# Performance work log

Hardware: AMD Instinct MI355X
Metric: run time of the kernel (lower is better)

## Reference

```python
import jax, jax.numpy as jnp
import numpy as np

EPS = 1e-9
TOP_K = 2


def setup_inputs() -> dict:
    key = jax.random.key(0)
    k = jax.random.split(key, 6)
    B, E, D_IN, D_MODEL, D_SEL = 16384, 8, 900, 512, 128
    return {
        "cycle_curve_data": jax.random.normal(k[0], (B, D_IN), jnp.float32),
        "logits": jax.random.normal(k[1], (B, E), jnp.float32),
        "moe_masks": jax.random.randint(k[2], (B, E), 0, 2, jnp.int32),
        "selection_embeddings": jax.random.normal(k[3], (B, E, D_SEL), jnp.float32),
        "W": jax.random.normal(k[4], (E, D_IN, D_MODEL), jnp.float32) / np.sqrt(D_IN).astype(np.float32),
        "b": jnp.zeros((E, D_MODEL), jnp.float32),
    }


def reference(cycle_curve_data, logits, moe_masks, selection_embeddings, W, b):
    B, E = logits.shape
    mask = (moe_masks == 1).astype(logits.dtype)  # [B, E]
    raw = jax.nn.softmax(logits, axis=1)          # [B, E]

    # inactive-expert mixture for selection embedding
    inactive = raw * (1.0 - mask)
    inactive = inactive / (jnp.sum(inactive, axis=1, keepdims=True) + EPS)
    selection_embedding = jnp.einsum("bes,be->bs", selection_embeddings, inactive)

    # active gates + top-k selection + renormalization
    active = raw * mask
    _, idx = jax.lax.top_k(active, TOP_K)                                  # [B, K]
    top_mask = jnp.sum(jax.nn.one_hot(idx, E, dtype=active.dtype), axis=1)  # [B, E]
    gates = active * top_mask
    gates = gates / (jnp.sum(gates, axis=1, keepdims=True) + EPS)

    # dense formulation of dispatch -> per-expert Linear -> weighted combine:
    # out[b] = sum_e gates[b,e] * (x[b] @ W[e] + b[e])
    expert_out = jnp.einsum("bd,edm->bem", cycle_curve_data, W) + b  # [B, E, D_model]
    final_out = jnp.einsum("bem,be->bm", expert_out, gates).astype(jnp.bfloat16)

    # guide loss (training-mode auxiliary loss)
    s = jnp.sum(raw * mask) / B
    guide_loss = (1.0 - s) * (1.0 - s)
    return final_out, guide_loss, selection_embedding
```

## Files before the change

### kernel.cpp

```cpp
#include <hip/hip_runtime.h>
#include <hip/hip_bf16.h>


#define B_ROWS 16384
#define DIN 900
#define DM 512
#define DSEL 128
#define KP 928
#define NKS 29
#define MAXT 192
#define EPSF 1e-9f

#define OUT_GUIDE (B_ROWS*DM)
#define OUT_SEL   (B_ROWS*DM + 1)

#define WS_COUNTS 0
#define WS_PART   512
#define WS_NT     768
#define WS_OFF    1024
#define WS_ENT    2048
#define WS_BB     9216
#define WS_PIDLR  25600
#define WS_GATEB  91136
#define WS_W8     222208
#define WS_ROWSS  746496
#define WS_WT     812032

#define FRSTRIDE 14848

typedef __attribute__((ext_vector_type(8))) short short8;
typedef __attribute__((ext_vector_type(8))) unsigned short ushort8;
typedef __attribute__((ext_vector_type(4))) float floatx4;

__device__ inline unsigned short f2bf(float v){
  union { __hip_bfloat16 h; unsigned short u; } c;
  c.h = __float2bfloat16(v);
  return c.u;
}
__device__ inline float bf2f(unsigned short u){
  union { unsigned int i; float f; } c;
  c.i = ((unsigned int)u) << 16;
  return c.f;
}
__device__ inline short8 pack8(float4 a, float4 b){
  union { ushort8 u; short8 s; } c;
  c.u[0]=f2bf(a.x); c.u[1]=f2bf(a.y); c.u[2]=f2bf(a.z); c.u[3]=f2bf(a.w);
  c.u[4]=f2bf(b.x); c.u[5]=f2bf(b.y); c.u[6]=f2bf(b.z); c.u[7]=f2bf(b.w);
  return c.s;
}

__global__ __launch_bounds__(256) void cvtw2_k(const float* __restrict__ W,
                                               unsigned short* __restrict__ wt2){
  __shared__ unsigned short lds[32][512];
  int t = threadIdx.x;
  int kc = blockIdx.x, e = blockIdx.y;
  for (int kk = 0; kk < 32; ++kk){
    int k = kc*32 + kk;
    if (k < DIN){
      const float* wr = W + ((size_t)e*DIN + k)*DM;
      lds[kk][t]       = f2bf(wr[t]);
      lds[kk][t + 256] = f2bf(wr[t + 256]);
    } else {
      lds[kk][t] = 0; lds[kk][t + 256] = 0;
    }
  }
  __syncthreads();
  int ncg = t >> 3, q = t & 7;
  unsigned short* ob = wt2 + (((size_t)e*32 + ncg)*29 + kc)*512;
  for (int i = 0; i < 8; ++i){
    int fb = i*64 + q*8;
    int col = fb >> 5, kk0 = fb & 31;
    ushort8 y;
    #pragma unroll
    for (int j = 0; j < 8; ++j) y[j] = lds[kk0 + j][ncg*16 + col];
    *((ushort8*)(ob + fb)) = y;
  }
}

__global__ __launch_bounds__(256) void gating_k(const float* __restrict__ logits,
                                                const int* __restrict__ masks,
                                                int* __restrict__ counts,
                                                float* __restrict__ partials,
                                                int* __restrict__ pidlr,
                                                float2* __restrict__ gatesb,
                                                float* __restrict__ w8,
                                                int* __restrict__ blockbase){
  __shared__ int hist[64];
  __shared__ float wsum[4];
  int t = threadIdx.x;
  if (t < 64) hist[t] = 0;
  __syncthreads();
  int b = blockIdx.x*256 + t;
  float4 l0 = *(const float4*)&logits[(size_t)b*8];
  float4 l1 = *(const float4*)&logits[(size_t)b*8 + 4];
  int4  m0 = *(const int4*)&masks[(size_t)b*8];
  int4  m1 = *(const int4*)&masks[(size_t)b*8 + 4];
  float raw[8] = {l0.x,l0.y,l0.z,l0.w,l1.x,l1.y,l1.z,l1.w};
  int   mk[8]  = {m0.x,m0.y,m0.z,m0.w,m1.x,m1.y,m1.z,m1.w};
  float mx = raw[0];
  for (int e = 1; e < 8; e++) mx = fmaxf(mx, raw[e]);
  float Z = 0.f;
  for (int e = 0; e < 8; e++){ raw[e] = expf(raw[e]-mx); Z += raw[e]; }
  float invZ = 1.f/Z;
  float act[8], ina[8]; float srm = 0.f, isum = 0.f;
  for (int e = 0; e < 8; e++){
    raw[e] *= invZ;
    if (mk[e] == 1){ act[e] = raw[e]; ina[e] = 0.f; srm += raw[e]; }
    else           { act[e] = 0.f;    ina[e] = raw[e]; isum += raw[e]; }
  }
  float v1 = -1.f, v2 = -1.f; int e1 = 0, e2 = 0;
  for (int e = 0; e < 8; e++){
    float a = act[e];
    if (a > v1){ v2 = v1; e2 = e1; v1 = a; e1 = e; }
    else if (a > v2){ v2 = a; e2 = e; }
  }
  float den = v1 + v2 + EPSF;
  float g1 = v1/den, g2 = v2/den;
  int lo, hi; float gl, gh;
  if (e1 < e2){ lo = e1; hi = e2; gl = g1; gh = g2; }
  else        { lo = e2; hi = e1; gl = g2; gh = g1; }
  int pid = lo*8 + hi;
  float invI = 1.f/(isum + EPSF);
  for (int e = 0; e < 8; e++) w8[(size_t)b*8 + e] = ina[e]*invI;
  gatesb[b] = make_float2(gl, gh);
  int lr = atomicAdd(&hist[pid], 1);
  pidlr[b] = pid | (lr << 8);
  float s = srm;
  for (int sft = 32; sft > 0; sft >>= 1) s += __shfl_down(s, sft, 64);
  if ((t & 63) == 0) wsum[t >> 6] = s;
  __syncthreads();
  if (t < 64){
    int c = hist[t];
    int base = 0;
    if (c > 0) base = atomicAdd(&counts[t], c);
    blockbase[blockIdx.x*64 + t] = base;
  }
  if (t == 0) partials[blockIdx.x] = wsum[0] + wsum[1] + wsum[2] + wsum[3];
}

__global__ __launch_bounds__(256) void selemb_k(const float* __restrict__ sel,
                                                const float* __restrict__ w8,
                                                const int* __restrict__ pidlr,
                                                const int* __restrict__ off,
                                                const int* __restrict__ blockbase,
                                                int* __restrict__ rows_s,
                                                float* __restrict__ out){
  int t = threadIdx.x;
  int b = blockIdx.x*2 + (t >> 7);
  int d = t & 127;
  if (d == 0){
    int pl = pidlr[b];
    int p = pl & 63;
    int lr = pl >> 8;
    rows_s[off[p] + blockbase[(b >> 8)*64 + p] + lr] = b;
  }
  const float* wr = w8 + (size_t)b*8;
  const float* sb = sel + (size_t)b*(8*DSEL);
  float a = 0.f;
  for (int e = 0; e < 8; e++) a += wr[e] * sb[e*DSEL + d];
  out[OUT_SEL + (size_t)b*DSEL + d] = a;
}

__global__ void worklist_k(const int* __restrict__ counts,
                           const float* __restrict__ partials,
                           int* __restrict__ off, int* __restrict__ ntp,
                           int4* __restrict__ entries,
                           float* __restrict__ out){
  int lane = threadIdx.x;
  int c = counts[lane];
  int sc = c;
  for (int s = 1; s < 64; s <<= 1){ int v = __shfl_up(sc, s, 64); if (lane >= s) sc += v; }
  int offp = sc - c;
  off[lane] = offp;
  int nt = (c + 127) >> 7;
  int snt = nt;
  for (int s = 1; s < 64; s <<= 1){ int v = __shfl_up(snt, s, 64); if (lane >= s) snt += v; }
  int tbase = snt - nt;
  int elo = lane >> 3, ehi = lane & 7;
  for (int j = 0; j < nt; ++j){
    int nr = c - j*128; if (nr > 128) nr = 128;
    entries[tbase + j] = make_int4(elo, ehi, offp + j*128, nr);
  }
  int tot = __shfl(snt, 63, 64);
  if (lane == 0) *ntp = tot;
  float p = partials[lane];
  for (int s = 32; s > 0; s >>= 1) p += __shfl_down(p, s, 64);
  if (lane == 0){
    float sv = p * (1.f/B_ROWS);
    float d = 1.f - sv;
    out[OUT_GUIDE] = d*d;
  }
}


#define LDRAW(kks) { \
  r0 = *(const float4*)(ap0 + (kks)*32); r1 = *(const float4*)(ap0 + (kks)*32 + 4); \
  r2 = *(const float4*)(ap1 + (kks)*32); r3 = *(const float4*)(ap1 + (kks)*32 + 4); \
  r4 = *(const float4*)(ap2 + (kks)*32); r5 = *(const float4*)(ap2 + (kks)*32 + 4); \
  r6 = *(const float4*)(ap3 + (kks)*32); r7 = *(const float4*)(ap3 + (kks)*32 + 4); }

#define LDRAW_TAIL() { \
  float4 z = make_float4(0.f,0.f,0.f,0.f); \
  float4 t0 = *(const float4*)(ap0 - quad*8 + 896); \
  float4 t1 = *(const float4*)(ap1 - quad*8 + 896); \
  float4 t2 = *(const float4*)(ap2 - quad*8 + 896); \
  float4 t3 = *(const float4*)(ap3 - quad*8 + 896); \
  r0 = (quad==0)? t0 : z; r1 = z; \
  r2 = (quad==0)? t1 : z; r3 = z; \
  r4 = (quad==0)? t2 : z; r5 = z; \
  r6 = (quad==0)? t3 : z; r7 = z; }

#define CVT(dst) { \
  dst##0 = pack8(r0, r1); dst##1 = pack8(r2, r3); \
  dst##2 = pack8(r4, r5); dst##3 = pack8(r6, r7); }

#define MF(afX, b, ei, nt) { \
  acc[ei][0][nt] = __builtin_amdgcn_mfma_f32_16x16x32_bf16(afX##0, b, acc[ei][0][nt], 0, 0, 0); \
  acc[ei][1][nt] = __builtin_amdgcn_mfma_f32_16x16x32_bf16(afX##1, b, acc[ei][1][nt], 0, 0, 0); \
  acc[ei][2][nt] = __builtin_amdgcn_mfma_f32_16x16x32_bf16(afX##2, b, acc[ei][2][nt], 0, 0, 0); \
  acc[ei][3][nt] = __builtin_amdgcn_mfma_f32_16x16x32_bf16(afX##3, b, acc[ei][3][nt], 0, 0, 0); }

#define STEP(afX, kks, LASTF) { \
  short8 b0n, b1n; \
   \
  b0n = *((const short8*)(bp0 + 1*FRSTRIDE + (kks)*512)); \
  b1n = *((const short8*)(bp1 + 1*FRSTRIDE + (kks)*512)); \
  MF(afX, b0c, 0, 0); MF(afX, b1c, 1, 0); b0c = b0n; b1c = b1n; \
   \
  b0n = *((const short8*)(bp0 + 2*FRSTRIDE + (kks)*512)); \
  b1n = *((const short8*)(bp1 + 2*FRSTRIDE + (kks)*512)); \
  MF(afX, b0c, 0, 1); MF(afX, b1c, 1, 1); b0c = b0n; b1c = b1n; \
   \
  b0n = *((const short8*)(bp0 + 3*FRSTRIDE + (kks)*512)); \
  b1n = *((const short8*)(bp1 + 3*FRSTRIDE + (kks)*512)); \
  MF(afX, b0c, 0, 2); MF(afX, b1c, 1, 2); b0c = b0n; b1c = b1n; \
   \
  if (!(LASTF)){ \
    b0n = *((const short8*)(bp0 + ((kks)+1)*512)); \
    b1n = *((const short8*)(bp1 + ((kks)+1)*512)); \
  } \
  MF(afX, b0c, 0, 3); MF(afX, b1c, 1, 3); b0c = b0n; b1c = b1n; }

__global__ __launch_bounds__(256, 2) void gemm_k(const float* __restrict__ xf,
                                                 const unsigned short* __restrict__ wt2,
                                                 const float* __restrict__ bias,
                                                 const int* __restrict__ ntp,
                                                 const int4* __restrict__ entries,
                                                 const int* __restrict__ rows_s,
                                                 const float2* __restrict__ gatesb,
                                                 float* __restrict__ out){
  int tile = blockIdx.x;
  if (tile >= *ntp) return;
  int4 ent = entries[tile];
  int elo = ent.x, ehi = ent.y, start = ent.z, nrows = ent.w;

  int t = threadIdx.x, lane = t & 63, wid = t >> 6;
  int wrow = wid >> 1, wcol = wid & 1;
  int quad = lane >> 4, l16 = lane & 15;
  int ncg0 = blockIdx.y*8 + wcol*4;

  const float* ap0; const float* ap1; const float* ap2; const float* ap3;
  {
    int rr, g;
    rr = wrow*64 + 0*16 + l16; g = (rr < nrows) ? rows_s[start + rr] : 0;
    ap0 = xf + (size_t)g*DIN + quad*8;
    rr = wrow*64 + 1*16 + l16; g = (rr < nrows) ? rows_s[start + rr] : 0;
    ap1 = xf + (size_t)g*DIN + quad*8;
    rr = wrow*64 + 2*16 + l16; g = (rr < nrows) ? rows_s[start + rr] : 0;
    ap2 = xf + (size_t)g*DIN + quad*8;
    rr = wrow*64 + 3*16 + l16; g = (rr < nrows) ? rows_s[start + rr] : 0;
    ap3 = xf + (size_t)g*DIN + quad*8;
  }
  const unsigned short* bp0 = wt2 + ((size_t)(elo*32 + ncg0)*29)*512 + l16*32 + quad*8;
  const unsigned short* bp1 = wt2 + ((size_t)(ehi*32 + ncg0)*29)*512 + l16*32 + quad*8;

  floatx4 acc[2][4][4];
  #pragma unroll
  for (int i = 0; i < 2; i++)
    #pragma unroll
    for (int j = 0; j < 4; j++)
      #pragma unroll
      for (int k = 0; k < 4; k++)
        #pragma unroll
        for (int r = 0; r < 4; r++) acc[i][j][k][r] = 0.f;

  float4 r0,r1,r2,r3,r4,r5,r6,r7;
  short8 afA0, afA1, afA2, afA3;
  short8 afB0, afB1, afB2, afB3;

  LDRAW(0);
  CVT(afA);
  short8 b0c = *((const short8*)(bp0));
  short8 b1c = *((const short8*)(bp1));

  for (int ks = 0; ks < 28; ks += 2){
    LDRAW(ks+1);
    STEP(afA, ks, false);
    CVT(afB);
    if (ks + 2 < 28){ LDRAW(ks+2); } else { LDRAW_TAIL(); }
    STEP(afB, ks+1, false);
    CVT(afA);
  }
  STEP(afA, 28, true);

  float blo[4], bhi[4];
  #pragma unroll
  for (int nt = 0; nt < 4; ++nt){
    int n = (ncg0 + nt)*16 + l16;
    blo[nt] = bias[elo*DM + n];
    bhi[nt] = bias[ehi*DM + n];
  }
  #pragma unroll
  for (int mt = 0; mt < 4; ++mt){
    #pragma unroll
    for (int r = 0; r < 4; ++r){
      int rr = wrow*64 + mt*16 + quad*4 + r;
      if (rr < nrows){
        int grow = rows_s[start + rr];
        float2 gg = gatesb[grow];
        float* orow = out + (size_t)grow*DM;
        #pragma unroll
        for (int nt = 0; nt < 4; ++nt){
          int n = (ncg0 + nt)*16 + l16;
          float v = gg.x*(acc[0][mt][nt][r] + blo[nt]) + gg.y*(acc[1][mt][nt][r] + bhi[nt]);
          orow[n] = bf2f(f2bf(v));
        }
      }
    }
  }
}

extern "C" void kernel_launch(void* const* d_in, const int* in_sizes, int n_in,
                              void* d_out, int out_size, void* d_ws, size_t ws_size,
                              hipStream_t stream){
  const float* x      = (const float*)d_in[0];
  const float* logits = (const float*)d_in[1];
  const int*   masks  = (const int*)d_in[2];
  const float* sel    = (const float*)d_in[3];
  const float* W      = (const float*)d_in[4];
  const float* bias   = (const float*)d_in[5];
  float* out = (float*)d_out;
  char* ws = (char*)d_ws;
  int*    counts   = (int*)(ws + WS_COUNTS);
  float*  partials = (float*)(ws + WS_PART);
  int*    ntp      = (int*)(ws + WS_NT);
  int*    off      = (int*)(ws + WS_OFF);
  int4*   entries  = (int4*)(ws + WS_ENT);
  int*    blockbase= (int*)(ws + WS_BB);
  int*    pidlr    = (int*)(ws + WS_PIDLR);
  float2* gatesb   = (float2*)(ws + WS_GATEB);
  float*  w8       = (float*)(ws + WS_W8);
  int*    rows_s   = (int*)(ws + WS_ROWSS);
  unsigned short* wt2 = (unsigned short*)(ws + WS_WT);

  hipMemsetAsync(ws, 0, 256, stream);
  cvtw2_k<<<dim3(29, 8), 256, 0, stream>>>(W, wt2);
  gating_k<<<B_ROWS/256, 256, 0, stream>>>(logits, masks, counts, partials, pidlr, gatesb, w8, blockbase);
  worklist_k<<<1, 64, 0, stream>>>(counts, partials, off, ntp, entries, out);
  selemb_k<<<B_ROWS/2, 256, 0, stream>>>(sel, w8, pidlr, off, blockbase, rows_s, out);
  gemm_k<<<dim3(MAXT, 4), 256, 0, stream>>>(x, wt2, bias, ntp, entries, rows_s, gatesb, out);
}
```

Baseline: 332.6 us.

## Stage A and B tiles through double-buffered LDS in expert GEMM

Rewrites the grouped-expert GEMM main loop. Each thread used to load its own A rows and B fragments straight from global memory, so waves sharing a tile fetched the same data separately. Now the block loads x rows (converted to bf16) and weight fragments cooperatively into padded, double-buffered shared memory, with one barrier per k-step, and each wave reads its MFMA operands from LDS. Gather indices and gates are cached in shared memory. This removes redundant global traffic, at the cost of LDS footprint, barrier stalls and possibly lower occupancy.

```diff
diff --git a/kernel.cpp b/kernel.cpp
--- a/kernel.cpp
+++ b/kernel.cpp
@@ -26,8 +26,6 @@
 #define WS_ROWSS  746496
 #define WS_WT     812032
 
-#define FRSTRIDE 14848
-
 typedef __attribute__((ext_vector_type(8))) short short8;
 typedef __attribute__((ext_vector_type(8))) unsigned short ushort8;
 typedef __attribute__((ext_vector_type(4))) float floatx4;
@@ -42,11 +40,11 @@
   c.i = ((unsigned int)u) << 16;
   return c.f;
 }
-__device__ inline short8 pack8(float4 a, float4 b){
-  union { ushort8 u; short8 s; } c;
-  c.u[0]=f2bf(a.x); c.u[1]=f2bf(a.y); c.u[2]=f2bf(a.z); c.u[3]=f2bf(a.w);
-  c.u[4]=f2bf(b.x); c.u[5]=f2bf(b.y); c.u[6]=f2bf(b.z); c.u[7]=f2bf(b.w);
-  return c.s;
+__device__ inline ushort8 pack8u(float4 a, float4 b){
+  ushort8 c;
+  c[0]=f2bf(a.x); c[1]=f2bf(a.y); c[2]=f2bf(a.z); c[3]=f2bf(a.w);
+  c[4]=f2bf(b.x); c[5]=f2bf(b.y); c[6]=f2bf(b.z); c[7]=f2bf(b.w);
+  return c;
 }
 
 __global__ __launch_bounds__(256) void cvtw2_k(const float* __restrict__ W,
@@ -193,53 +191,38 @@
 }
 
 
-#define LDRAW(kks) { \
-  r0 = *(const float4*)(ap0 + (kks)*32); r1 = *(const float4*)(ap0 + (kks)*32 + 4); \
-  r2 = *(const float4*)(ap1 + (kks)*32); r3 = *(const float4*)(ap1 + (kks)*32 + 4); \
-  r4 = *(const float4*)(ap2 + (kks)*32); r5 = *(const float4*)(ap2 + (kks)*32 + 4); \
-  r6 = *(const float4*)(ap3 + (kks)*32); r7 = *(const float4*)(ap3 + (kks)*32 + 4); }
-
-#define LDRAW_TAIL() { \
-  float4 z = make_float4(0.f,0.f,0.f,0.f); \
-  float4 t0 = *(const float4*)(ap0 - quad*8 + 896); \
-  float4 t1 = *(const float4*)(ap1 - quad*8 + 896); \
-  float4 t2 = *(const float4*)(ap2 - quad*8 + 896); \
-  float4 t3 = *(const float4*)(ap3 - quad*8 + 896); \
-  r0 = (quad==0)? t0 : z; r1 = z; \
-  r2 = (quad==0)? t1 : z; r3 = z; \
-  r4 = (quad==0)? t2 : z; r5 = z; \
-  r6 = (quad==0)? t3 : z; r7 = z; }
-
-#define CVT(dst) { \
-  dst##0 = pack8(r0, r1); dst##1 = pack8(r2, r3); \
-  dst##2 = pack8(r4, r5); dst##3 = pack8(r6, r7); }
-
-#define MF(afX, b, ei, nt) { \
-  acc[ei][0][nt] = __builtin_amdgcn_mfma_f32_16x16x32_bf16(afX##0, b, acc[ei][0][nt], 0, 0, 0); \
-  acc[ei][1][nt] = __builtin_amdgcn_mfma_f32_16x16x32_bf16(afX##1, b, acc[ei][1][nt], 0, 0, 0); \
-  acc[ei][2][nt] = __builtin_amdgcn_mfma_f32_16x16x32_bf16(afX##2, b, acc[ei][2][nt], 0, 0, 0); \
-  acc[ei][3][nt] = __builtin_amdgcn_mfma_f32_16x16x32_bf16(afX##3, b, acc[ei][3][nt], 0, 0, 0); }
-
-#define STEP(afX, kks, LASTF) { \
-  short8 b0n, b1n; \
-   \
-  b0n = *((const short8*)(bp0 + 1*FRSTRIDE + (kks)*512)); \
-  b1n = *((const short8*)(bp1 + 1*FRSTRIDE + (kks)*512)); \
-  MF(afX, b0c, 0, 0); MF(afX, b1c, 1, 0); b0c = b0n; b1c = b1n; \
-   \
-  b0n = *((const short8*)(bp0 + 2*FRSTRIDE + (kks)*512)); \
-  b1n = *((const short8*)(bp1 + 2*FRSTRIDE + (kks)*512)); \
-  MF(afX, b0c, 0, 1); MF(afX, b1c, 1, 1); b0c = b0n; b1c = b1n; \
-   \
-  b0n = *((const short8*)(bp0 + 3*FRSTRIDE + (kks)*512)); \
-  b1n = *((const short8*)(bp1 + 3*FRSTRIDE + (kks)*512)); \
-  MF(afX, b0c, 0, 2); MF(afX, b1c, 1, 2); b0c = b0n; b1c = b1n; \
-   \
-  if (!(LASTF)){ \
-    b0n = *((const short8*)(bp0 + ((kks)+1)*512)); \
-    b1n = *((const short8*)(bp1 + ((kks)+1)*512)); \
-  } \
-  MF(afX, b0c, 0, 3); MF(afX, b1c, 1, 3); b0c = b0n; b1c = b1n; }
+#define ALOAD(kk) { \
+  if ((kk) < 28){ \
+    const float4* p = (const float4*)(xrow + (kk)*32); \
+    a0 = p[0]; a1 = p[1]; a2 = p[2]; a3 = p[3]; \
+  } else { \
+    float tmp[16]; \
+    _Pragma("unroll") \
+    for (int j = 0; j < 16; ++j){ \
+      int k = (kk)*32 + skc*16 + j; \
+      tmp[j] = (k < DIN) ? xrow[(kk)*32 + j] : 0.f; \
+    } \
+    a0 = make_float4(tmp[0],tmp[1],tmp[2],tmp[3]); \
+    a1 = make_float4(tmp[4],tmp[5],tmp[6],tmp[7]); \
+    a2 = make_float4(tmp[8],tmp[9],tmp[10],tmp[11]); \
+    a3 = make_float4(tmp[12],tmp[13],tmp[14],tmp[15]); \
+  } }
+
+#define BLOAD(kk) { \
+  bw0 = *((const ushort8*)(bg0 + (size_t)(kk)*512)); \
+  bw1 = *((const ushort8*)(bg1 + (size_t)(kk)*512)); \
+  bw2 = *((const ushort8*)(bg2 + (size_t)(kk)*512)); \
+  bw3 = *((const ushort8*)(bg3 + (size_t)(kk)*512)); }
+
+#define AWRITE(buf) { \
+  *((ushort8*)&as_[buf][srow*40 + skc*16])     = pack8u(a0, a1); \
+  *((ushort8*)&as_[buf][srow*40 + skc*16 + 8]) = pack8u(a2, a3); }
+
+#define BWRITE(buf) { \
+  *((ushort8*)&bs_[buf][bl0]) = bw0; \
+  *((ushort8*)&bs_[buf][bl1]) = bw1; \
+  *((ushort8*)&bs_[buf][bl2]) = bw2; \
+  *((ushort8*)&bs_[buf][bl3]) = bw3; }
 
 __global__ __launch_bounds__(256, 2) void gemm_k(const float* __restrict__ xf,
                                                  const unsigned short* __restrict__ wt2,
@@ -254,25 +237,48 @@
   int4 ent = entries[tile];
   int elo = ent.x, ehi = ent.y, start = ent.z, nrows = ent.w;
 
-  int t = threadIdx.x, lane = t & 63, wid = t >> 6;
+  __shared__ __align__(16) unsigned short as_[2][128*40];
+  __shared__ __align__(16) unsigned short bs_[2][16*16*40];
+  __shared__ int   gidx_s[128];
+  __shared__ float glo_s[128];
+  __shared__ float ghi_s[128];
+
+  int t = threadIdx.x;
+  if (t < 128){
+    if (t < nrows){
+      int g = rows_s[start + t];
+      gidx_s[t] = g;
+      float2 gg = gatesb[g];
+      glo_s[t] = gg.x; ghi_s[t] = gg.y;
+    } else { gidx_s[t] = -1; glo_s[t] = 0.f; ghi_s[t] = 0.f; }
+  }
+  __syncthreads();
+
+  int lane = t & 63, wid = t >> 6;
   int wrow = wid >> 1, wcol = wid & 1;
   int quad = lane >> 4, l16 = lane & 15;
-  int ncg0 = blockIdx.y*8 + wcol*4;
-
-  const float* ap0; const float* ap1; const float* ap2; const float* ap3;
+
+  int srow = t >> 1, skc = t & 1;
+  int sg = gidx_s[srow];
+  const float* xrow = xf + (size_t)(sg >= 0 ? sg : 0)*DIN + skc*16;
+
+  int bcol = (t & 63) >> 2, bq = t & 3;
+  const unsigned short* bg0; const unsigned short* bg1;
+  const unsigned short* bg2; const unsigned short* bg3;
+  int bl0, bl1, bl2, bl3;
   {
-    int rr, g;
-    rr = wrow*64 + 0*16 + l16; g = (rr < nrows) ? rows_s[start + rr] : 0;
-    ap0 = xf + (size_t)g*DIN + quad*8;
-    rr = wrow*64 + 1*16 + l16; g = (rr < nrows) ? rows_s[start + rr] : 0;
-    ap1 = xf + (size_t)g*DIN + quad*8;
-    rr = wrow*64 + 2*16 + l16; g = (rr < nrows) ? rows_s[start + rr] : 0;
-    ap2 = xf + (size_t)g*DIN + quad*8;
-    rr = wrow*64 + 3*16 + l16; g = (rr < nrows) ? rows_s[start + rr] : 0;
-    ap3 = xf + (size_t)g*DIN + quad*8;
-  }
-  const unsigned short* bp0 = wt2 + ((size_t)(elo*32 + ncg0)*29)*512 + l16*32 + quad*8;
-  const unsigned short* bp1 = wt2 + ((size_t)(ehi*32 + ncg0)*29)*512 + l16*32 + quad*8;
+    int u0 = t, u1 = 256 + t, u2 = 512 + t, u3 = 768 + t;
+    int j0 = (u0 >> 6) & 7, j1 = (u1 >> 6) & 7, j2 = (u2 >> 6) & 7, j3 = (u3 >> 6) & 7;
+    int goff = (t & 63)*8;
+    bg0 = wt2 + ((size_t)(elo*32 + blockIdx.y*8 + j0)*29)*512 + goff;
+    bg1 = wt2 + ((size_t)(elo*32 + blockIdx.y*8 + j1)*29)*512 + goff;
+    bg2 = wt2 + ((size_t)(ehi*32 + blockIdx.y*8 + j2)*29)*512 + goff;
+    bg3 = wt2 + ((size_t)(ehi*32 + blockIdx.y*8 + j3)*29)*512 + goff;
+    bl0 = ((0*8 + j0)*16 + bcol)*40 + bq*8;
+    bl1 = ((0*8 + j1)*16 + bcol)*40 + bq*8;
+    bl2 = ((1*8 + j2)*16 + bcol)*40 + bq*8;
+    bl3 = ((1*8 + j3)*16 + bcol)*40 + bq*8;
+  }
 
   floatx4 acc[2][4][4];
   #pragma unroll
@@ -284,29 +290,42 @@
         #pragma unroll
         for (int r = 0; r < 4; r++) acc[i][j][k][r] = 0.f;
 
-  float4 r0,r1,r2,r3,r4,r5,r6,r7;
-  short8 afA0, afA1, afA2, afA3;
-  short8 afB0, afB1, afB2, afB3;
-
-  LDRAW(0);
-  CVT(afA);
-  short8 b0c = *((const short8*)(bp0));
-  short8 b1c = *((const short8*)(bp1));
-
-  for (int ks = 0; ks < 28; ks += 2){
-    LDRAW(ks+1);
-    STEP(afA, ks, false);
-    CVT(afB);
-    if (ks + 2 < 28){ LDRAW(ks+2); } else { LDRAW_TAIL(); }
-    STEP(afB, ks+1, false);
-    CVT(afA);
-  }
-  STEP(afA, 28, true);
-
+  float4 a0, a1, a2, a3;
+  ushort8 bw0, bw1, bw2, bw3;
+
+  ALOAD(0); BLOAD(0);
+  AWRITE(0); BWRITE(0);
+  __syncthreads();
+
+  for (int ks = 0; ks < NKS; ++ks){
+    int cur = ks & 1;
+    int nk = ks + 1;
+    if (nk < NKS){ ALOAD(nk); BLOAD(nk); }
+
+    short8 af[4];
+    #pragma unroll
+    for (int mt = 0; mt < 4; ++mt)
+      af[mt] = *((const short8*)&as_[cur][(wrow*64 + mt*16 + l16)*40 + quad*8]);
+    #pragma unroll
+    for (int e = 0; e < 2; ++e){
+      #pragma unroll
+      for (int nt = 0; nt < 4; ++nt){
+        short8 bfr = *((const short8*)&bs_[cur][((e*8 + wcol*4 + nt)*16 + l16)*40 + quad*8]);
+        #pragma unroll
+        for (int mt = 0; mt < 4; ++mt)
+          acc[e][mt][nt] = __builtin_amdgcn_mfma_f32_16x16x32_bf16(af[mt], bfr, acc[e][mt][nt], 0, 0, 0);
+      }
+    }
+
+    if (nk < NKS){ AWRITE(cur ^ 1); BWRITE(cur ^ 1); }
+    __syncthreads();
+  }
+
+  int colbase = blockIdx.y*128 + wcol*64;
   float blo[4], bhi[4];
   #pragma unroll
   for (int nt = 0; nt < 4; ++nt){
-    int n = (ncg0 + nt)*16 + l16;
+    int n = colbase + nt*16 + l16;
     blo[nt] = bias[elo*DM + n];
     bhi[nt] = bias[ehi*DM + n];
   }
@@ -315,13 +334,13 @@
     #pragma unroll
     for (int r = 0; r < 4; ++r){
       int rr = wrow*64 + mt*16 + quad*4 + r;
-      if (rr < nrows){
-        int grow = rows_s[start + rr];
+      int grow = gidx_s[rr];
+      if (grow >= 0){
         float2 gg = gatesb[grow];
         float* orow = out + (size_t)grow*DM;
         #pragma unroll
         for (int nt = 0; nt < 4; ++nt){
-          int n = (ncg0 + nt)*16 + l16;
+          int n = colbase + nt*16 + l16;
           float v = gg.x*(acc[0][mt][nt][r] + blo[nt]) + gg.y*(acc[1][mt][nt][r] + bhi[nt]);
           orow[n] = bf2f(f2bf(v));
         }
```

Result: faster. 286.2 us (-14.0%).
